# Performance work log

Measured on AMD Instinct MI355X. Metric: run time of the kernel, lower is better.

The kernel has to match this reference:

```python
import jax, jax.numpy as jnp
import numpy as np

PATCH = 16
STRIDE = 8  # patch_size - overlap

def setup_inputs() -> dict:
    key = jax.random.key(0)
    x = jax.random.normal(key, (16, 3, 512, 512), dtype=jnp.float32)
    return {"x": x, "k_neighbors": 8}

def reference(x, k_neighbors):
    B, C, H, W = x.shape
    p, s = PATCH, STRIDE
    nh = (H - p) // s + 1
    nw = (W - p) // s + 1
    N = nh * nw
    # F.unfold equivalent: feature dim ordered (C, kh, kw), then transpose(1,2)
    patches = jax.lax.conv_general_dilated_patches(
        x, filter_shape=(p, p), window_strides=(s, s), padding='VALID')  # [B, C*p*p, nh, nw]
    patches = patches.reshape(B, C * p * p, N).transpose(0, 2, 1)  # [B, N, C*p*p]
    # grid positions [(i, j)] row-major, same order as the python double loop
    ii, jj = jnp.meshgrid(jnp.arange(nh), jnp.arange(nw), indexing='ij')
    pos = jnp.stack([ii.ravel(), jj.ravel()], axis=1).astype(jnp.float32)  # [N, 2]
    positions = jnp.broadcast_to(pos[None], (B, N, 2))
    k = min(int(k_neighbors) + 1, N)
    def knn(posb):
        # squared euclidean distance preserves the ordering of cdist(p=2)
        d2 = jnp.sum((posb[:, None, :] - posb[None, :, :]) ** 2, axis=-1)  # [N, N]
        _, idx = jax.lax.top_k(-d2, k)  # k smallest distances
        tgt = idx[:, 1:]  # drop self (distance 0)
        src = jnp.broadcast_to(jnp.arange(N)[:, None], tgt.shape)
        return jnp.stack([src.ravel(), tgt.ravel()], axis=0)  # [2, N*k_neighbors]
    edge_index = jax.vmap(knn)(positions)  # [B, 2, N*k_neighbors]
    return patches, positions, edge_index
```

## Files before the change

### kernel.cpp

```cpp
#include <hip/hip_runtime.h>

#define BB      16
#define CH      3
#define HH      512
#define WW      512
#define NH      63
#define NW      63
#define NN      3969
#define FDIM    768
#define EDGES   31752

#define PATCHES_ELEMS  (BB * NN * FDIM)
#define POS_ELEMS      (BB * NN * 2)

#define PE_THREADS   (BB * NN)
#define PE_BLOCKS    ((PE_THREADS + 255) / 256)
#define PATCH_BLOCKS (BB * NH * CH)

typedef float  f4 __attribute__((ext_vector_type(4)));
typedef float  f2 __attribute__((ext_vector_type(2)));

__global__ __launch_bounds__(256) void fused_kernel(const float* __restrict__ x,
                                                    float* __restrict__ out) {
    unsigned bid = blockIdx.x;

    if (bid >= PE_BLOCKS) {
        unsigned pb = bid - PE_BLOCKS;
        unsigned c  = pb % CH;
        unsigned bi = pb / CH;
        unsigned i  = bi % NH;
        unsigned b  = bi / NH;
        unsigned tid = threadIdx.x;

        __shared__ float lds[16 * 512];

        const float* base = x + ((size_t)(b * CH + c) * HH + i * 8u) * WW;

        typedef const __attribute__((address_space(1))) void* gas_p;
        typedef __attribute__((address_space(3))) void*       las_p;
#pragma unroll
        for (unsigned u = 0; u < 8; ++u) {
            unsigned f4id = u * 256u + tid;
            __builtin_amdgcn_global_load_lds((gas_p)(const void*)(base + f4id * 4u),
                                             (las_p)(void*)(lds + f4id * 4u),
                                             16, 0, 0);
        }
        __syncthreads();

        unsigned lane = tid & 63u;
        unsigned wave = tid >> 6;
        unsigned row  = (lane >> 2) << 9;
        unsigned coff = (lane & 3u) << 2;
        float* obase = out + ((size_t)(b * NN + i * NW) * FDIM) + c * 256u + (lane << 2);

#pragma unroll
        for (unsigned jj = 0; jj < 16; ++jj) {
            unsigned j = jj * 4u + wave;
            if (j < NW) {
                const f4 v = *reinterpret_cast<const f4*>(lds + row + j * 8u + coff);
                __builtin_nontemporal_store(
                    v, reinterpret_cast<f4*>(obase + (size_t)j * FDIM));
            }
        }
    } else {
        unsigned g = bid * 256u + threadIdx.x;
        if (g >= PE_THREADS) return;
        unsigned n = g % NN;
        unsigned b = g / NN;
        int i = (int)(n / NW);
        int j = (int)(n - (unsigned)i * NW);

        *reinterpret_cast<f2*>(out + PATCHES_ELEMS + (size_t)(b * NN + n) * 2) =
            f2{(float)i, (float)j};

        unsigned best[9];
#pragma unroll
        for (int s = 0; s < 9; ++s) best[s] = 0xFFFFFFFFu;
        for (int di = -2; di <= 2; ++di) {
            int ni = i + di;
            if (ni < 0 || ni >= NH) continue;
            for (int dj = -2; dj <= 2; ++dj) {
                int nj = j + dj;
                if (nj < 0 || nj >= NW) continue;
                unsigned key = ((unsigned)(di * di + dj * dj) << 12)
                             | (unsigned)(ni * NW + nj);
#pragma unroll
                for (int s = 0; s < 9; ++s) {
                    if (key < best[s]) { unsigned tmp = best[s]; best[s] = key; key = tmp; }
                }
            }
        }

        float src_f = (float)n;
        f4 s4 = {src_f, src_f, src_f, src_f};
        f4 t0 = {(float)(best[1] & 0xFFFu), (float)(best[2] & 0xFFFu),
                 (float)(best[3] & 0xFFFu), (float)(best[4] & 0xFFFu)};
        f4 t1 = {(float)(best[5] & 0xFFFu), (float)(best[6] & 0xFFFu),
                 (float)(best[7] & 0xFFFu), (float)(best[8] & 0xFFFu)};

        float* ebase = out + PATCHES_ELEMS + POS_ELEMS + (size_t)b * 2 * EDGES;
        *reinterpret_cast<f4*>(ebase + (size_t)n * 8)             = s4;
        *reinterpret_cast<f4*>(ebase + (size_t)n * 8 + 4)         = s4;
        *reinterpret_cast<f4*>(ebase + EDGES + (size_t)n * 8)     = t0;
        *reinterpret_cast<f4*>(ebase + EDGES + (size_t)n * 8 + 4) = t1;
    }
}

extern "C" void kernel_launch(void* const* d_in, const int* in_sizes, int n_in,
                              void* d_out, int out_size, void* d_ws, size_t ws_size,
                              hipStream_t stream) {
    const float* x = (const float*)d_in[0];
    float* out     = (float*)d_out;
    fused_kernel<<<PE_BLOCKS + PATCH_BLOCKS, 256, 0, stream>>>(x, out);
}
```

Before: 232.7 us.

## Retile patch extraction by column quarter, covering all channels in each block

After: 235.4 us. About the same (+1.2%).

```diff
diff --git a/kernel.cpp b/kernel.cpp
--- a/kernel.cpp
+++ b/kernel.cpp
@@ -15,7 +15,12 @@
 
 #define PE_THREADS   (BB * NN)
 #define PE_BLOCKS    ((PE_THREADS + 255) / 256)
-#define PATCH_BLOCKS (BB * NH * CH)
+#define NJQ          4
+#define PATCH_BLOCKS (BB * NH * NJQ)
+
+#define ROWF4   34
+#define SLOTS   1632
+#define SLOTS_P 1792
 
 typedef float  f4 __attribute__((ext_vector_type(4)));
 typedef float  f2 __attribute__((ext_vector_type(2)));
@@ -26,40 +31,51 @@
 
     if (bid >= PE_BLOCKS) {
         unsigned pb = bid - PE_BLOCKS;
-        unsigned c  = pb % CH;
-        unsigned bi = pb / CH;
+        unsigned jq = pb & 3u;
+        unsigned bi = pb >> 2;
         unsigned i  = bi % NH;
         unsigned b  = bi / NH;
         unsigned tid = threadIdx.x;
 
-        __shared__ float lds[16 * 512];
-
-        const float* base = x + ((size_t)(b * CH + c) * HH + i * 8u) * WW;
+        __shared__ float lds[SLOTS_P * 4];
 
         typedef const __attribute__((address_space(1))) void* gas_p;
         typedef __attribute__((address_space(3))) void*       las_p;
+
+        const float* xb = x + (size_t)b * (CH * HH * WW) + (size_t)(i * 8u) * WW;
+
 #pragma unroll
-        for (unsigned u = 0; u < 8; ++u) {
-            unsigned f4id = u * 256u + tid;
-            __builtin_amdgcn_global_load_lds((gas_p)(const void*)(base + f4id * 4u),
-                                             (las_p)(void*)(lds + f4id * 4u),
+        for (unsigned it = 0; it < 7; ++it) {
+            unsigned s  = it * 256u + tid;
+            unsigned se = s < (SLOTS - 1) ? s : (SLOTS - 1);
+            unsigned r  = se / ROWF4;
+            unsigned k  = se - r * ROWF4;
+            unsigned col = jq * 128u + (k << 2);
+            col = col < 508u ? col : 508u;
+            const float* src = xb + ((size_t)(r >> 4) * (HH * WW))
+                                  + (size_t)(r & 15u) * WW + col;
+            __builtin_amdgcn_global_load_lds((gas_p)(const void*)src,
+                                             (las_p)(void*)(lds + s * 4u),
                                              16, 0, 0);
         }
         __syncthreads();
 
-        unsigned lane = tid & 63u;
-        unsigned wave = tid >> 6;
-        unsigned row  = (lane >> 2) << 9;
-        unsigned coff = (lane & 3u) << 2;
-        float* obase = out + ((size_t)(b * NN + i * NW) * FDIM) + c * 256u + (lane << 2);
-
+        unsigned npat   = (jq == 3) ? 15u : 16u;
+        unsigned nslots = npat * 192u;
+        float* obase = out + (size_t)(b * NN + i * NW + jq * 16u) * FDIM;
 #pragma unroll
-        for (unsigned jj = 0; jj < 16; ++jj) {
-            unsigned j = jj * 4u + wave;
-            if (j < NW) {
-                const f4 v = *reinterpret_cast<const f4*>(lds + row + j * 8u + coff);
+        for (unsigned it = 0; it < 12; ++it) {
+            unsigned t = it * 256u + tid;
+            if (t < nslots) {
+                unsigned p   = t / 192u;
+                unsigned f4i = t - p * 192u;
+                unsigned c   = f4i >> 6;
+                unsigned di  = (f4i >> 2) & 15u;
+                unsigned dj  = (f4i & 3u) << 2;
+                const f4 v = *reinterpret_cast<const f4*>(
+                    lds + ((c * 16u + di) * 136u + p * 8u + dj));
                 __builtin_nontemporal_store(
-                    v, reinterpret_cast<f4*>(obase + (size_t)j * FDIM));
+                    v, reinterpret_cast<f4*>(obase + (size_t)t * 4));
             }
         }
     } else {
```
